# Kernel tuning notes

Hardware: AMD Instinct MI355X
Metric: run time of the kernel (lower is better)

Reference implementation:

```python
import jax, jax.numpy as jnp
import numpy as np

N = 100000   # nodes
E = 3200000  # edges
D = 128      # in_channels
H = 128      # subhiddens
O = 128      # out_channels
S = 2048     # subgraphs
EPS = 1e-5


def _glorot(k, shape):
    lim = np.sqrt(6.0 / (shape[0] + shape[1])).astype(np.float32)
    return jax.random.uniform(k, shape, jnp.float32, -lim, lim)


def setup_inputs() -> dict:
    key = jax.random.key(0)
    ks = jax.random.split(key, 8)
    x = jax.random.normal(ks[0], (N, D), jnp.float32)
    edge_index = jax.random.randint(ks[1], (2, E), 0, N, dtype=jnp.int32)
    node_to_subgraph = jnp.sort(jax.random.randint(ks[2], (N,), 0, S, dtype=jnp.int32))
    return {
        "x": x,
        "edge_index": edge_index,
        "node_to_subgraph": node_to_subgraph,
        "W1": _glorot(ks[3], (D, H)), "b1": jnp.zeros((H,), jnp.float32),
        "g1": jnp.ones((H,), jnp.float32), "be1": jnp.zeros((H,), jnp.float32),
        "W2": _glorot(ks[4], (H, H)), "b2": jnp.zeros((H,), jnp.float32),
        "g2": jnp.ones((H,), jnp.float32), "be2": jnp.zeros((H,), jnp.float32),
        "W3": _glorot(ks[5], (H, O)), "b3": jnp.zeros((O,), jnp.float32),
    }


def _gcn_conv(x, W, b, row, col, norm):
    # PyG GCNConv: out[col] += norm * (x @ W)[row], then + bias.
    xw = x @ W                                    # [N+?, d] -> [N, d_out]
    msg = xw[row] * norm[:, None]                 # gather over source nodes
    out = jax.ops.segment_sum(msg, col, num_segments=N)
    return out + b


def _bn_relu(x, g, be):
    # BatchNorm1d (training-mode batch stats, biased var) + ReLU
    mean = jnp.mean(x, axis=0)
    var = jnp.mean(jnp.square(x - mean), axis=0)
    return jax.nn.relu((x - mean) * jax.lax.rsqrt(var + EPS) * g + be)


def reference(x, edge_index, node_to_subgraph, W1, b1, g1, be1, W2, b2, g2, be2, W3, b3):
    # GCN symmetric norm with self-loops, shared across the 3 convs.
    loops = jnp.arange(N, dtype=edge_index.dtype)
    row = jnp.concatenate([edge_index[0], loops])  # source
    col = jnp.concatenate([edge_index[1], loops])  # target (aggregation)
    deg = jax.ops.segment_sum(jnp.ones_like(col, dtype=x.dtype), col, num_segments=N)
    dinv = jnp.where(deg > 0, jax.lax.rsqrt(deg), 0.0)
    norm = dinv[row] * dinv[col]

    h1 = _bn_relu(_gcn_conv(x, W1, b1, row, col, norm), g1, be1)   # dropout is no-op in eval
    h2 = _bn_relu(_gcn_conv(h1, W2, b2, row, col, norm), g2, be2)
    h3 = jax.nn.relu(_gcn_conv(h2, W3, b3, row, col, norm))

    cat = jnp.concatenate([h1, h2, h3], axis=-1)                   # [N, 2H+O]
    return jax.ops.segment_max(cat, node_to_subgraph, num_segments=S)  # gmp -> [S, 2H+O]
```

## Files before the change

### kernel.cpp

```cpp
#include <hip/hip_runtime.h>
#include <hip/hip_fp16.h>

#define NN 100000
#define NE 3200000
#define DF 128
#define SG 2048
#define OUTC 384
#define EPS 1e-5f

#define NBUK 800
#define BNODES 125
#define CAP 4608
#define TILE 8192
#define LDSTRIDE 136

typedef _Float16 f16x8 __attribute__((ext_vector_type(8)));
typedef float f32x16 __attribute__((ext_vector_type(16)));

__global__ void k_prepW(const float* __restrict__ W1, const float* __restrict__ W2,
                        const float* __restrict__ W3, __half* __restrict__ WT) {
    const float* W = blockIdx.x == 0 ? W1 : (blockIdx.x == 1 ? W2 : W3);
    __half* out = WT + blockIdx.x * 16384;
    for (int i = threadIdx.x; i < 16384; i += 256) {
        int k = i >> 7, n = i & 127;
        out[n * 128 + k] = __float2half(W[i]);
    }
}

__global__ __launch_bounds__(256) void k_bucketA(const int* __restrict__ erow,
                                                 const int* __restrict__ ecol,
                                                 int* __restrict__ gcur,
                                                 int* __restrict__ packed) {
    __shared__ int hist[1024];
    __shared__ int loff[1024];
    __shared__ int gch[1024];
    __shared__ int cur[1024];
    __shared__ int psum[256];
    int t = threadIdx.x;
    hist[t] = 0; hist[t + 256] = 0; hist[t + 512] = 0; hist[t + 768] = 0;
    __syncthreads();
    int e0 = blockIdx.x * TILE;
    for (int i = t; i < TILE && e0 + i < NE; i += 256) {
        int c = ecol[e0 + i];
        atomicAdd(&hist[c / BNODES], 1);
    }
    __syncthreads();
    int h0 = hist[4 * t], h1 = hist[4 * t + 1], h2 = hist[4 * t + 2], h3 = hist[4 * t + 3];
    int s = h0 + h1 + h2 + h3;
    psum[t] = s; __syncthreads();
    for (int st = 1; st < 256; st <<= 1) {
        int a = (t >= st) ? psum[t - st] : 0;
        __syncthreads();
        psum[t] += a;
        __syncthreads();
    }
    int base = psum[t] - s;
    loff[4 * t] = base;
    loff[4 * t + 1] = base + h0;
    loff[4 * t + 2] = base + h0 + h1;
    loff[4 * t + 3] = base + h0 + h1 + h2;
#pragma unroll
    for (int j = 0; j < 4; ++j) {
        int b = 4 * t + j;
        if (b < NBUK) {
            int c = hist[b];
            gch[b] = c ? atomicAdd(&gcur[b], c) : 0;
            cur[b] = loff[b];
        }
    }
    __syncthreads();
    for (int i = t; i < TILE && e0 + i < NE; i += 256) {
        int c = ecol[e0 + i];
        int r = erow[e0 + i];
        int b = c / BNODES;
        int lc = c - b * BNODES;
        int p = atomicAdd(&cur[b], 1);
        int rank = p - loff[b];
        if (gch[b] + rank < CAP) packed[b * CAP + gch[b] + rank] = r | (lc << 17);
    }
}

__global__ __launch_bounds__(256) void k_csrB(int* __restrict__ rows,
                                              const int* __restrict__ gcur,
                                              int* __restrict__ begs, int* __restrict__ ends,
                                              float* __restrict__ dinv) {
    __shared__ int lin[CAP];
    __shared__ int hist[128], off[128], cur[128], psc[128];
    int b = blockIdx.x, t = threadIdx.x;
    int cnt = gcur[b]; if (cnt > CAP) cnt = CAP;
    int base = b * CAP;
    for (int i = t; i < cnt; i += 256) lin[i] = rows[base + i];
    if (t < 128) hist[t] = 0;
    __syncthreads();
    for (int i = t; i < cnt; i += 256) atomicAdd(&hist[lin[i] >> 17], 1);
    __syncthreads();
    if (t < 128) psc[t] = hist[t];
    __syncthreads();
    for (int st = 1; st < 128; st <<= 1) {
        int a = 0;
        if (t < 128 && t >= st) a = psc[t - st];
        __syncthreads();
        if (t < 128) psc[t] += a;
        __syncthreads();
    }
    if (t < 128) { off[t] = psc[t] - hist[t]; cur[t] = off[t]; }
    __syncthreads();
    if (t < BNODES) {
        int n = b * BNODES + t;
        int c = hist[t];
        int bg = base + off[t];
        begs[n] = bg;
        ends[n] = bg + c;
        dinv[n] = rsqrtf((float)(c + 1));
    }
    __syncthreads();
    for (int i = t; i < cnt; i += 256) {
        int w = lin[i];
        int lc = w >> 17;
        int p = atomicAdd(&cur[lc], 1);
        rows[base + p] = w & 0x1FFFF;
    }
}

__global__ __launch_bounds__(256, 2) void k_gemm16(const __half* __restrict__ A,
                                                   const __half* __restrict__ WTg,
                                                   const float* __restrict__ dinv,
                                                   __half* __restrict__ C) {
    __shared__ _Float16 Wl[128 * LDSTRIDE];
    int tid = threadIdx.x;
    for (int ch = tid; ch < 2048; ch += 256) {
        int n = ch >> 4, seg = ch & 15;
        *(uint4*)&Wl[n * LDSTRIDE + seg * 8] = *(const uint4*)(WTg + n * 128 + seg * 8);
    }
    __syncthreads();
    int wave = tid >> 6, lane = tid & 63;
    int l31 = lane & 31, lhi = lane >> 5;
    int rowbase = blockIdx.x * 256 + wave * 64;
    f32x16 acc[2][4];
#pragma unroll
    for (int rt = 0; rt < 2; ++rt)
#pragma unroll
        for (int nt = 0; nt < 4; ++nt)
#pragma unroll
            for (int i = 0; i < 16; ++i) acc[rt][nt][i] = 0.f;
    int r0 = rowbase + l31;      if (r0 >= NN) r0 = NN - 1;
    int r1 = rowbase + 32 + l31; if (r1 >= NN) r1 = NN - 1;
    const f16x8* A0 = (const f16x8*)(A + (size_t)r0 * 128);
    const f16x8* A1 = (const f16x8*)(A + (size_t)r1 * 128);
#pragma unroll
    for (int ks = 0; ks < 8; ++ks) {
        f16x8 a0 = A0[ks * 2 + lhi];
        f16x8 a1 = A1[ks * 2 + lhi];
#pragma unroll
        for (int nt = 0; nt < 4; ++nt) {
            f16x8 b = *(const f16x8*)&Wl[(nt * 32 + l31) * LDSTRIDE + ks * 16 + lhi * 8];
            acc[0][nt] = __builtin_amdgcn_mfma_f32_32x32x16_f16(a0, b, acc[0][nt], 0, 0, 0);
            acc[1][nt] = __builtin_amdgcn_mfma_f32_32x32x16_f16(a1, b, acc[1][nt], 0, 0, 0);
        }
    }
#pragma unroll
    for (int rt = 0; rt < 2; ++rt) {
#pragma unroll
        for (int r = 0; r < 16; ++r) {
            int row = rowbase + rt * 32 + (r & 3) + 8 * (r >> 2) + 4 * lhi;
            if (row < NN) {
                float sc = dinv[row];
                size_t cb = (size_t)row * 128 + l31;
                C[cb]      = __float2half(acc[rt][0][r] * sc);
                C[cb + 32] = __float2half(acc[rt][1][r] * sc);
                C[cb + 64] = __float2half(acc[rt][2][r] * sc);
                C[cb + 96] = __float2half(acc[rt][3][r] * sc);
            }
        }
    }
}

__global__ __launch_bounds__(256, 2) void k_gemm32(const float* __restrict__ A,
                                                   const __half* __restrict__ WTg,
                                                   const float* __restrict__ dinv,
                                                   __half* __restrict__ C) {
    __shared__ _Float16 Wl[128 * LDSTRIDE];
    int tid = threadIdx.x;
    for (int ch = tid; ch < 2048; ch += 256) {
        int n = ch >> 4, seg = ch & 15;
        *(uint4*)&Wl[n * LDSTRIDE + seg * 8] = *(const uint4*)(WTg + n * 128 + seg * 8);
    }
    __syncthreads();
    int wave = tid >> 6, lane = tid & 63;
    int l31 = lane & 31, lhi = lane >> 5;
    int rowbase = blockIdx.x * 256 + wave * 64;
    f32x16 acc[2][4];
#pragma unroll
    for (int rt = 0; rt < 2; ++rt)
#pragma unroll
        for (int nt = 0; nt < 4; ++nt)
#pragma unroll
            for (int i = 0; i < 16; ++i) acc[rt][nt][i] = 0.f;
    int r0 = rowbase + l31;      if (r0 >= NN) r0 = NN - 1;
    int r1 = rowbase + 32 + l31; if (r1 >= NN) r1 = NN - 1;
    const float* A0 = A + (size_t)r0 * 128;
    const float* A1 = A + (size_t)r1 * 128;
#pragma unroll
    for (int ks = 0; ks < 8; ++ks) {
        int koff = ks * 16 + lhi * 8;
        float4 f0 = *(const float4*)(A0 + koff);
        float4 f1 = *(const float4*)(A0 + koff + 4);
        float4 g0 = *(const float4*)(A1 + koff);
        float4 g1 = *(const float4*)(A1 + koff + 4);
        f16x8 a0, a1;
        a0[0] = (_Float16)f0.x; a0[1] = (_Float16)f0.y; a0[2] = (_Float16)f0.z; a0[3] = (_Float16)f0.w;
        a0[4] = (_Float16)f1.x; a0[5] = (_Float16)f1.y; a0[6] = (_Float16)f1.z; a0[7] = (_Float16)f1.w;
        a1[0] = (_Float16)g0.x; a1[1] = (_Float16)g0.y; a1[2] = (_Float16)g0.z; a1[3] = (_Float16)g0.w;
        a1[4] = (_Float16)g1.x; a1[5] = (_Float16)g1.y; a1[6] = (_Float16)g1.z; a1[7] = (_Float16)g1.w;
#pragma unroll
        for (int nt = 0; nt < 4; ++nt) {
            f16x8 b = *(const f16x8*)&Wl[(nt * 32 + l31) * LDSTRIDE + ks * 16 + lhi * 8];
            acc[0][nt] = __builtin_amdgcn_mfma_f32_32x32x16_f16(a0, b, acc[0][nt], 0, 0, 0);
            acc[1][nt] = __builtin_amdgcn_mfma_f32_32x32x16_f16(a1, b, acc[1][nt], 0, 0, 0);
        }
    }
#pragma unroll
    for (int rt = 0; rt < 2; ++rt) {
#pragma unroll
        for (int r = 0; r < 16; ++r) {
            int row = rowbase + rt * 32 + (r & 3) + 8 * (r >> 2) + 4 * lhi;
            if (row < NN) {
                float sc = dinv[row];
                size_t cb = (size_t)row * 128 + l31;
                C[cb]      = __float2half(acc[rt][0][r] * sc);
                C[cb + 32] = __float2half(acc[rt][1][r] * sc);
                C[cb + 64] = __float2half(acc[rt][2][r] * sc);
                C[cb + 96] = __float2half(acc[rt][3][r] * sc);
            }
        }
    }
}

__device__ __forceinline__ void accum8(float* acc, uint4 v) {
    float2 f;
    f = __half22float2(*(__half2*)&v.x); acc[0] += f.x; acc[1] += f.y;
    f = __half22float2(*(__half2*)&v.y); acc[2] += f.x; acc[3] += f.y;
    f = __half22float2(*(__half2*)&v.z); acc[4] += f.x; acc[5] += f.y;
    f = __half22float2(*(__half2*)&v.w); acc[6] += f.x; acc[7] += f.y;
}
__device__ __forceinline__ void accum8w(float* acc, uint4 v, float w) {
    float2 f;
    f = __half22float2(*(__half2*)&v.x); acc[0] = fmaf(w, f.x, acc[0]); acc[1] = fmaf(w, f.y, acc[1]);
    f = __half22float2(*(__half2*)&v.y); acc[2] = fmaf(w, f.x, acc[2]); acc[3] = fmaf(w, f.y, acc[3]);
    f = __half22float2(*(__half2*)&v.z); acc[4] = fmaf(w, f.x, acc[4]); acc[5] = fmaf(w, f.y, acc[5]);
    f = __half22float2(*(__half2*)&v.w); acc[6] = fmaf(w, f.x, acc[6]); acc[7] = fmaf(w, f.y, acc[7]);
}

__global__ __launch_bounds__(256) void k_aggh(const __half* __restrict__ XWh,
                                              const int* __restrict__ begs,
                                              const int* __restrict__ ends,
                                              const int* __restrict__ rows,
                                              const float* __restrict__ dinv,
                                              __half* __restrict__ outh) {
    int n = (blockIdx.x * 256 + threadIdx.x) >> 6;
    int lane = threadIdx.x & 63;
    if (n >= NN) return;
    int quad = lane >> 4, li = lane & 15;
    float dn = dinv[n];
    int beg = begs[n], end = ends[n];
    const uint4* XW4 = (const uint4*)XWh;
    float acc[8] = {};
    if (quad == 0) {
        uint4 sv = XW4[(size_t)n * 16 + li];
        accum8(acc, sv);
    }
    int e = beg;
    for (; e + 32 <= end; e += 32) {
        int r0 = rows[e + quad];
        int r1 = rows[e + 4 + quad];
        int r2 = rows[e + 8 + quad];
        int r3 = rows[e + 12 + quad];
        int r4 = rows[e + 16 + quad];
        int r5 = rows[e + 20 + quad];
        int r6 = rows[e + 24 + quad];
        int r7 = rows[e + 28 + quad];
        uint4 v0 = XW4[(size_t)r0 * 16 + li];
        uint4 v1 = XW4[(size_t)r1 * 16 + li];
        uint4 v2 = XW4[(size_t)r2 * 16 + li];
        uint4 v3 = XW4[(size_t)r3 * 16 + li];
        uint4 v4 = XW4[(size_t)r4 * 16 + li];
        uint4 v5 = XW4[(size_t)r5 * 16 + li];
        uint4 v6 = XW4[(size_t)r6 * 16 + li];
        uint4 v7 = XW4[(size_t)r7 * 16 + li];
        accum8(acc, v0); accum8(acc, v1); accum8(acc, v2); accum8(acc, v3);
        accum8(acc, v4); accum8(acc, v5); accum8(acc, v6); accum8(acc, v7);
    }
    for (; e + 16 <= end; e += 16) {
        int r0 = rows[e + quad];
        int r1 = rows[e + 4 + quad];
        int r2 = rows[e + 8 + quad];
        int r3 = rows[e + 12 + quad];
        uint4 v0 = XW4[(size_t)r0 * 16 + li];
        uint4 v1 = XW4[(size_t)r1 * 16 + li];
        uint4 v2 = XW4[(size_t)r2 * 16 + li];
        uint4 v3 = XW4[(size_t)r3 * 16 + li];
        accum8(acc, v0); accum8(acc, v1); accum8(acc, v2); accum8(acc, v3);
    }
    for (; e < end; e += 4) {
        int idx = e + quad;
        int valid = idx < end;
        int r = valid ? rows[idx] : rows[end - 1];
        uint4 v = XW4[(size_t)r * 16 + li];
        accum8w(acc, v, valid ? 1.0f : 0.0f);
    }
#pragma unroll
    for (int j = 0; j < 8; ++j) {
        acc[j] += __shfl_xor(acc[j], 16, 64);
        acc[j] += __shfl_xor(acc[j], 32, 64);
    }
    if (quad == 0) {
        __half2 h0 = __floats2half2_rn(acc[0] * dn, acc[1] * dn);
        __half2 h1 = __floats2half2_rn(acc[2] * dn, acc[3] * dn);
        __half2 h2 = __floats2half2_rn(acc[4] * dn, acc[5] * dn);
        __half2 h3 = __floats2half2_rn(acc[6] * dn, acc[7] * dn);
        uint4 st;
        st.x = *(unsigned int*)&h0;
        st.y = *(unsigned int*)&h1;
        st.z = *(unsigned int*)&h2;
        st.w = *(unsigned int*)&h3;
        *(uint4*)(outh + (size_t)n * 128 + li * 8) = st;
    }
}

__global__ void k_stats(const __half* __restrict__ buf, float* __restrict__ sums) {
    int c = threadIdx.x & 127;
    int rg = threadIdx.x >> 7;
    float s = 0.f, q = 0.f;
    for (int r = blockIdx.x * 2 + rg; r < NN; r += gridDim.x * 2) {
        float v = __half2float(buf[(size_t)r * 128 + c]);
        s += v; q += v * v;
    }
    __shared__ float sh[512];
    sh[threadIdx.x] = s;
    sh[256 + threadIdx.x] = q;
    __syncthreads();
    if (threadIdx.x < 128) {
        s = sh[threadIdx.x] + sh[threadIdx.x + 128];
        q = sh[256 + threadIdx.x] + sh[256 + threadIdx.x + 128];
        atomicAdd(&sums[threadIdx.x], s);
        atomicAdd(&sums[128 + threadIdx.x], q);
    }
}

__global__ void k_finstats(const float* __restrict__ sums, const float* __restrict__ g,
                           const float* __restrict__ be, float* __restrict__ scsh) {
    int c = threadIdx.x;
    float mean = sums[c] * (1.0f / NN);
    float var = sums[128 + c] * (1.0f / NN) - mean * mean;
    float inv = rsqrtf(var + EPS) * g[c];
    scsh[c] = inv;
    scsh[128 + c] = be[c] - mean * inv;
}

__global__ void k_bnmax(__half* __restrict__ buf, const float* __restrict__ scsh,
                        const int* __restrict__ n2s,
                        unsigned int* __restrict__ outmax, int colOff) {
    int c = threadIdx.x & 127;
    int rg = threadIdx.x >> 7;
    int n0 = blockIdx.x * 64;
    int nEnd = n0 + 64; if (nEnd > NN) nEnd = NN;
    float sc = scsh[c], sh = scsh[128 + c];
    int cur = -1; float runmax = 0.f;
    for (int n = n0 + rg; n < nEnd; n += 2) {
        float v = fmaxf(__half2float(buf[(size_t)n * 128 + c]) * sc + sh, 0.f);
        buf[(size_t)n * 128 + c] = __float2half(v);
        int sg = n2s[n];
        if (sg != cur) {
            if (cur >= 0) atomicMax(&outmax[cur * OUTC + colOff + c], __float_as_uint(runmax));
            cur = sg; runmax = v;
        } else {
            runmax = fmaxf(runmax, v);
        }
    }
    if (cur >= 0) atomicMax(&outmax[cur * OUTC + colOff + c], __float_as_uint(runmax));
}

__global__ void k_biasmax(const __half* __restrict__ buf, const float* __restrict__ b3,
                          const int* __restrict__ n2s,
                          unsigned int* __restrict__ outmax, int colOff) {
    int c = threadIdx.x & 127;
    int rg = threadIdx.x >> 7;
    int n0 = blockIdx.x * 64;
    int nEnd = n0 + 64; if (nEnd > NN) nEnd = NN;
    float bias = b3[c];
    int cur = -1; float runmax = 0.f;
    for (int n = n0 + rg; n < nEnd; n += 2) {
        float v = fmaxf(__half2float(buf[(size_t)n * 128 + c]) + bias, 0.f);
        int sg = n2s[n];
        if (sg != cur) {
            if (cur >= 0) atomicMax(&outmax[cur * OUTC + colOff + c], __float_as_uint(runmax));
            cur = sg; runmax = v;
        } else {
            runmax = fmaxf(runmax, v);
        }
    }
    if (cur >= 0) atomicMax(&outmax[cur * OUTC + colOff + c], __float_as_uint(runmax));
}

extern "C" void kernel_launch(void* const* d_in, const int* in_sizes, int n_in,
                              void* d_out, int out_size, void* d_ws, size_t ws_size,
                              hipStream_t stream) {
    const float* x   = (const float*)d_in[0];
    const int*   ei  = (const int*)d_in[1];
    const int*   n2s = (const int*)d_in[2];
    const float* W1  = (const float*)d_in[3];
    const float* g1  = (const float*)d_in[5];
    const float* be1 = (const float*)d_in[6];
    const float* W2  = (const float*)d_in[7];
    const float* g2  = (const float*)d_in[9];
    const float* be2 = (const float*)d_in[10];
    const float* W3  = (const float*)d_in[11];
    const float* b3  = (const float*)d_in[12];

    __half* H    = (__half*)d_ws;
    __half* XWh  = H + (size_t)NN * 128;
    __half* WT   = XWh + (size_t)NN * 128;
    int* rows    = (int*)(WT + 3 * 16384);
    int* begs    = rows + (size_t)NBUK * CAP;
    int* ends    = begs + NN;
    float* dinv  = (float*)(ends + NN);
    int* gcur    = (int*)(dinv + NN);
    float* sums  = (float*)(gcur + NBUK);
    float* scsh  = sums + 512;

    const int* erow = ei;
    const int* ecol = ei + NE;

    hipMemsetAsync(gcur, 0, (NBUK + 512) * sizeof(int), stream);
    hipMemsetAsync(d_out, 0, (size_t)out_size * sizeof(float), stream);

    k_prepW<<<3, 256, 0, stream>>>(W1, W2, W3, WT);
    int nbA = (NE + TILE - 1) / TILE;
    k_bucketA<<<nbA, 256, 0, stream>>>(erow, ecol, gcur, rows);
    k_csrB<<<NBUK, 256, 0, stream>>>(rows, gcur, begs, ends, dinv);

    unsigned int* outmax = (unsigned int*)d_out;
    int nbSeg = (NN + 63) / 64;
    int nbG = (NN + 255) / 256;

    k_gemm32<<<nbG, 256, 0, stream>>>(x, WT, dinv, XWh);
    k_aggh<<<NN / 4, 256, 0, stream>>>(XWh, begs, ends, rows, dinv, H);
    k_stats<<<512, 256, 0, stream>>>(H, sums);
    k_finstats<<<1, 128, 0, stream>>>(sums, g1, be1, scsh);
    k_bnmax<<<nbSeg, 256, 0, stream>>>(H, scsh, n2s, outmax, 0);

    k_gemm16<<<nbG, 256, 0, stream>>>(H, WT + 16384, dinv, XWh);
    k_aggh<<<NN / 4, 256, 0, stream>>>(XWh, begs, ends, rows, dinv, H);
    k_stats<<<512, 256, 0, stream>>>(H, sums + 256);
    k_finstats<<<1, 128, 0, stream>>>(sums + 256, g2, be2, scsh + 256);
    k_bnmax<<<nbSeg, 256, 0, stream>>>(H, scsh + 256, n2s, outmax, 128);

    k_gemm16<<<nbG, 256, 0, stream>>>(H, WT + 32768, dinv, XWh);
    k_aggh<<<NN / 4, 256, 0, stream>>>(XWh, begs, ends, rows, dinv, H);
    k_biasmax<<<nbSeg, 256, 0, stream>>>(H, b3, n2s, outmax, 256);
}
```

Before: 735.1 us.

## Pad CSR segments to 4, vectorize index loads, persistent aggregation grid, fold finstats

Result: no change. 731.2 us (-0.5%).

```diff
diff --git a/kernel.cpp b/kernel.cpp
--- a/kernel.cpp
+++ b/kernel.cpp
@@ -10,7 +10,7 @@
 
 #define NBUK 800
 #define BNODES 125
-#define CAP 4608
+#define CAP 5120
 #define TILE 8192
 #define LDSTRIDE 136
 
@@ -94,7 +94,8 @@
     __syncthreads();
     for (int i = t; i < cnt; i += 256) atomicAdd(&hist[lin[i] >> 17], 1);
     __syncthreads();
-    if (t < 128) psc[t] = hist[t];
+    int pc = 0;
+    if (t < 128) { pc = (hist[t] + 3) & ~3; psc[t] = pc; }
     __syncthreads();
     for (int st = 1; st < 128; st <<= 1) {
         int a = 0;
@@ -103,7 +104,7 @@
         if (t < 128) psc[t] += a;
         __syncthreads();
     }
-    if (t < 128) { off[t] = psc[t] - hist[t]; cur[t] = off[t]; }
+    if (t < 128) { off[t] = psc[t] - pc; cur[t] = off[t]; }
     __syncthreads();
     if (t < BNODES) {
         int n = b * BNODES + t;
@@ -112,13 +113,16 @@
         begs[n] = bg;
         ends[n] = bg + c;
         dinv[n] = rsqrtf((float)(c + 1));
+        int pad = (c + 3) & ~3;
+        for (int p = c; p < pad; ++p)
+            if (off[t] + p < CAP) rows[base + off[t] + p] = 0;
     }
     __syncthreads();
     for (int i = t; i < cnt; i += 256) {
         int w = lin[i];
         int lc = w >> 17;
         int p = atomicAdd(&cur[lc], 1);
-        rows[base + p] = w & 0x1FFFF;
+        if (p < CAP) rows[base + p] = w & 0x1FFFF;
     }
 }
 
@@ -251,79 +255,79 @@
     f = __half22float2(*(__half2*)&v.w); acc[6] = fmaf(w, f.x, acc[6]); acc[7] = fmaf(w, f.y, acc[7]);
 }
 
+#define AGG_BLOCKS 4096
 __global__ __launch_bounds__(256) void k_aggh(const __half* __restrict__ XWh,
                                               const int* __restrict__ begs,
                                               const int* __restrict__ ends,
                                               const int* __restrict__ rows,
                                               const float* __restrict__ dinv,
                                               __half* __restrict__ outh) {
-    int n = (blockIdx.x * 256 + threadIdx.x) >> 6;
+    int wid = (blockIdx.x * 256 + threadIdx.x) >> 6;
     int lane = threadIdx.x & 63;
-    if (n >= NN) return;
     int quad = lane >> 4, li = lane & 15;
-    float dn = dinv[n];
-    int beg = begs[n], end = ends[n];
     const uint4* XW4 = (const uint4*)XWh;
-    float acc[8] = {};
-    if (quad == 0) {
-        uint4 sv = XW4[(size_t)n * 16 + li];
-        accum8(acc, sv);
-    }
-    int e = beg;
-    for (; e + 32 <= end; e += 32) {
-        int r0 = rows[e + quad];
-        int r1 = rows[e + 4 + quad];
-        int r2 = rows[e + 8 + quad];
-        int r3 = rows[e + 12 + quad];
-        int r4 = rows[e + 16 + quad];
-        int r5 = rows[e + 20 + quad];
-        int r6 = rows[e + 24 + quad];
-        int r7 = rows[e + 28 + quad];
-        uint4 v0 = XW4[(size_t)r0 * 16 + li];
-        uint4 v1 = XW4[(size_t)r1 * 16 + li];
-        uint4 v2 = XW4[(size_t)r2 * 16 + li];
-        uint4 v3 = XW4[(size_t)r3 * 16 + li];
-        uint4 v4 = XW4[(size_t)r4 * 16 + li];
-        uint4 v5 = XW4[(size_t)r5 * 16 + li];
-        uint4 v6 = XW4[(size_t)r6 * 16 + li];
-        uint4 v7 = XW4[(size_t)r7 * 16 + li];
-        accum8(acc, v0); accum8(acc, v1); accum8(acc, v2); accum8(acc, v3);
-        accum8(acc, v4); accum8(acc, v5); accum8(acc, v6); accum8(acc, v7);
-    }
-    for (; e + 16 <= end; e += 16) {
-        int r0 = rows[e + quad];
-        int r1 = rows[e + 4 + quad];
-        int r2 = rows[e + 8 + quad];
-        int r3 = rows[e + 12 + quad];
-        uint4 v0 = XW4[(size_t)r0 * 16 + li];
-        uint4 v1 = XW4[(size_t)r1 * 16 + li];
-        uint4 v2 = XW4[(size_t)r2 * 16 + li];
-        uint4 v3 = XW4[(size_t)r3 * 16 + li];
-        accum8(acc, v0); accum8(acc, v1); accum8(acc, v2); accum8(acc, v3);
-    }
-    for (; e < end; e += 4) {
-        int idx = e + quad;
-        int valid = idx < end;
-        int r = valid ? rows[idx] : rows[end - 1];
-        uint4 v = XW4[(size_t)r * 16 + li];
-        accum8w(acc, v, valid ? 1.0f : 0.0f);
-    }
-#pragma unroll
-    for (int j = 0; j < 8; ++j) {
-        acc[j] += __shfl_xor(acc[j], 16, 64);
-        acc[j] += __shfl_xor(acc[j], 32, 64);
-    }
-    if (quad == 0) {
-        __half2 h0 = __floats2half2_rn(acc[0] * dn, acc[1] * dn);
-        __half2 h1 = __floats2half2_rn(acc[2] * dn, acc[3] * dn);
-        __half2 h2 = __floats2half2_rn(acc[4] * dn, acc[5] * dn);
-        __half2 h3 = __floats2half2_rn(acc[6] * dn, acc[7] * dn);
-        uint4 st;
-        st.x = *(unsigned int*)&h0;
-        st.y = *(unsigned int*)&h1;
-        st.z = *(unsigned int*)&h2;
-        st.w = *(unsigned int*)&h3;
-        *(uint4*)(outh + (size_t)n * 128 + li * 8) = st;
+    for (int n = wid; n < NN; n += AGG_BLOCKS * 4) {
+        float dn = dinv[n];
+        int beg = begs[n], end = ends[n];
+        float acc[8] = {};
+        if (quad == 0) {
+            uint4 sv = XW4[(size_t)n * 16 + li];
+            accum8(acc, sv);
+        }
+        int e = beg;
+        for (; e + 32 <= end; e += 32) {
+            int4 ia = *(const int4*)(rows + e + 4 * quad);
+            int4 ib = *(const int4*)(rows + e + 16 + 4 * quad);
+            uint4 v0 = XW4[(size_t)ia.x * 16 + li];
+            uint4 v1 = XW4[(size_t)ia.y * 16 + li];
+            uint4 v2 = XW4[(size_t)ia.z * 16 + li];
+            uint4 v3 = XW4[(size_t)ia.w * 16 + li];
+            uint4 v4 = XW4[(size_t)ib.x * 16 + li];
+            uint4 v5 = XW4[(size_t)ib.y * 16 + li];
+            uint4 v6 = XW4[(size_t)ib.z * 16 + li];
+            uint4 v7 = XW4[(size_t)ib.w * 16 + li];
+            accum8(acc, v0); accum8(acc, v1); accum8(acc, v2); accum8(acc, v3);
+            accum8(acc, v4); accum8(acc, v5); accum8(acc, v6); accum8(acc, v7);
+        }
+        for (; e + 16 <= end; e += 16) {
+            int4 ia = *(const int4*)(rows + e + 4 * quad);
+            uint4 v0 = XW4[(size_t)ia.x * 16 + li];
+            uint4 v1 = XW4[(size_t)ia.y * 16 + li];
+            uint4 v2 = XW4[(size_t)ia.z * 16 + li];
+            uint4 v3 = XW4[(size_t)ia.w * 16 + li];
+            accum8(acc, v0); accum8(acc, v1); accum8(acc, v2); accum8(acc, v3);
+        }
+        if (e < end) {
+            int rem = end - e;
+            int qb = 4 * quad;
+            int4 it = make_int4(0, 0, 0, 0);
+            if (qb < rem) it = *(const int4*)(rows + e + qb);
+            uint4 v0 = XW4[(size_t)it.x * 16 + li];
+            uint4 v1 = XW4[(size_t)it.y * 16 + li];
+            uint4 v2 = XW4[(size_t)it.z * 16 + li];
+            uint4 v3 = XW4[(size_t)it.w * 16 + li];
+            accum8w(acc, v0, (qb + 0 < rem) ? 1.f : 0.f);
+            accum8w(acc, v1, (qb + 1 < rem) ? 1.f : 0.f);
+            accum8w(acc, v2, (qb + 2 < rem) ? 1.f : 0.f);
+            accum8w(acc, v3, (qb + 3 < rem) ? 1.f : 0.f);
+        }
+#pragma unroll
+        for (int j = 0; j < 8; ++j) {
+            acc[j] += __shfl_xor(acc[j], 16, 64);
+            acc[j] += __shfl_xor(acc[j], 32, 64);
+        }
+        if (quad == 0) {
+            __half2 h0 = __floats2half2_rn(acc[0] * dn, acc[1] * dn);
+            __half2 h1 = __floats2half2_rn(acc[2] * dn, acc[3] * dn);
+            __half2 h2 = __floats2half2_rn(acc[4] * dn, acc[5] * dn);
+            __half2 h3 = __floats2half2_rn(acc[6] * dn, acc[7] * dn);
+            uint4 st;
+            st.x = *(unsigned int*)&h0;
+            st.y = *(unsigned int*)&h1;
+            st.z = *(unsigned int*)&h2;
+            st.w = *(unsigned int*)&h3;
+            *(uint4*)(outh + (size_t)n * 128 + li * 8) = st;
+        }
     }
 }
 
@@ -347,24 +351,17 @@
     }
 }
 
-__global__ void k_finstats(const float* __restrict__ sums, const float* __restrict__ g,
-                           const float* __restrict__ be, float* __restrict__ scsh) {
-    int c = threadIdx.x;
-    float mean = sums[c] * (1.0f / NN);
-    float var = sums[128 + c] * (1.0f / NN) - mean * mean;
-    float inv = rsqrtf(var + EPS) * g[c];
-    scsh[c] = inv;
-    scsh[128 + c] = be[c] - mean * inv;
-}
-
-__global__ void k_bnmax(__half* __restrict__ buf, const float* __restrict__ scsh,
+__global__ void k_bnmax(__half* __restrict__ buf, const float* __restrict__ sums,
+                        const float* __restrict__ g, const float* __restrict__ be,
                         const int* __restrict__ n2s,
                         unsigned int* __restrict__ outmax, int colOff) {
     int c = threadIdx.x & 127;
     int rg = threadIdx.x >> 7;
     int n0 = blockIdx.x * 64;
     int nEnd = n0 + 64; if (nEnd > NN) nEnd = NN;
-    float sc = scsh[c], sh = scsh[128 + c];
+    float mean = sums[c] * (1.0f / NN);
+    float inv = rsqrtf(sums[128 + c] * (1.0f / NN) - mean * mean + EPS) * g[c];
+    float sc = inv, sh = be[c] - mean * inv;
     int cur = -1; float runmax = 0.f;
     for (int n = n0 + rg; n < nEnd; n += 2) {
         float v = fmaxf(__half2float(buf[(size_t)n * 128 + c]) * sc + sh, 0.f);
@@ -426,7 +423,6 @@
     float* dinv  = (float*)(ends + NN);
     int* gcur    = (int*)(dinv + NN);
     float* sums  = (float*)(gcur + NBUK);
-    float* scsh  = sums + 512;
 
     const int* erow = ei;
     const int* ecol = ei + NE;
@@ -444,18 +440,16 @@
     int nbG = (NN + 255) / 256;
 
     k_gemm32<<<nbG, 256, 0, stream>>>(x, WT, dinv, XWh);
-    k_aggh<<<NN / 4, 256, 0, stream>>>(XWh, begs, ends, rows, dinv, H);
+    k_aggh<<<AGG_BLOCKS, 256, 0, stream>>>(XWh, begs, ends, rows, dinv, H);
     k_stats<<<512, 256, 0, stream>>>(H, sums);
-    k_finstats<<<1, 128, 0, stream>>>(sums, g1, be1, scsh);
-    k_bnmax<<<nbSeg, 256, 0, stream>>>(H, scsh, n2s, outmax, 0);
+    k_bnmax<<<nbSeg, 256, 0, stream>>>(H, sums, g1, be1, n2s, outmax, 0);
 
     k_gemm16<<<nbG, 256, 0, stream>>>(H, WT + 16384, dinv, XWh);
-    k_aggh<<<NN / 4, 256, 0, stream>>>(XWh, begs, ends, rows, dinv, H);
+    k_aggh<<<AGG_BLOCKS, 256, 0, stream>>>(XWh, begs, ends, rows, dinv, H);
     k_stats<<<512, 256, 0, stream>>>(H, sums + 256);
-    k_finstats<<<1, 128, 0, stream>>>(sums + 256, g2, be2, scsh + 256);
-    k_bnmax<<<nbSeg, 256, 0, stream>>>(H, scsh + 256, n2s, outmax, 128);
+    k_bnmax<<<nbSeg, 256, 0, stream>>>(H, sums + 256, g2, be2, n2s, outmax, 128);
 
     k_gemm16<<<nbG, 256, 0, stream>>>(H, WT + 32768, dinv, XWh);
-    k_aggh<<<NN / 4, 256, 0, stream>>>(XWh, begs, ends, rows, dinv, H);
+    k_aggh<<<AGG_BLOCKS, 256, 0, stream>>>(XWh, begs, ends, rows, dinv, H);
     k_biasmax<<<nbSeg, 256, 0, stream>>>(H, b3, n2s, outmax, 256);
 }
```
